# Optimization experiments

Hardware: AMD Instinct MI355X
Metric: run time of the kernel (lower is better)

Reference implementation:

```python
import jax, jax.numpy as jnp
import numpy as np

VEC, H, B, S = 768, 256, 64, 512


def setup_inputs() -> dict:
    key = jax.random.key(0)
    ks = jax.random.split(key, 8)
    sc = 0.02
    return {
        "output_1": jax.random.normal(ks[0], (B, S, VEC), dtype=jnp.float32),
        "output_2": jax.random.normal(ks[1], (B, S, VEC), dtype=jnp.float32),
        "mlp_w": jax.random.normal(ks[2], (H, VEC), dtype=jnp.float32) * sc,
        "mlp_b": jnp.zeros((H,), dtype=jnp.float32),
        "fd_w": jax.random.normal(ks[3], (H, 2 * H), dtype=jnp.float32) * sc,
        "fd_b": jnp.zeros((H,), dtype=jnp.float32),
        "ff_w": jax.random.normal(ks[4], (1, H), dtype=jnp.float32) * sc,
        "ff_b": jnp.zeros((1,), dtype=jnp.float32),
    }


def reference(output_1, output_2, mlp_w, mlp_b, fd_w, fd_b, ff_w, ff_b):
    # eval-mode forward of Bert_coss
    o1 = jax.nn.relu(output_1 @ mlp_w.T + mlp_b)        # [B,S,H]
    o2 = jax.nn.relu(output_2 @ mlp_w.T + mlp_b)        # [B,S,H]
    o1_doc = jnp.mean(o1, axis=1)                        # [B,H]
    o2_doc = jnp.mean(o2, axis=1)                        # [B,H]
    h = jax.nn.relu(jnp.concatenate([o1_doc, o2_doc], axis=1) @ fd_w.T + fd_b)
    out = jax.nn.sigmoid(jnp.squeeze(h @ ff_w.T + ff_b))  # [B]
    # append doc vectors as an extra token
    o1e = jnp.concatenate([o1, o1_doc[:, None, :]], axis=1)  # [B,S+1,H]
    o2e = jnp.concatenate([o2, o2_doc[:, None, :]], axis=1)  # [B,S+1,H]
    # graph_match: scores + softmax over dim=1; only last column is used downstream
    a = jnp.einsum('bsh,bth->bst', o1e, o2e)             # [B,S+1,S+1]
    a_x = jax.nn.softmax(a, axis=1)
    att = a_x[:, :, -1].T                                # [S+1,B]
    att = jnp.concatenate([att[:-1], out[None, :]], axis=0)  # [S+1,B]
    return att
```

## Files before the change

### kernel.cpp

```cpp
#include <hip/hip_runtime.h>
#include <hip/hip_bf16.h>
#include <math.h>

#define B_ 64
#define S_ 512
#define VEC_ 768
#define H_ 256
#define M_ (B_*S_)

typedef float floatx4 __attribute__((ext_vector_type(4)));
typedef __bf16 bf16x8 __attribute__((ext_vector_type(8)));
typedef __bf16 bf16x4 __attribute__((ext_vector_type(4)));

#define STRIDE 40

__global__ __launch_bounds__(256) void prep_kernel(
    const float* __restrict__ mlp_w, __bf16* __restrict__ wbf, float* __restrict__ sums)
{
  const int bid = blockIdx.x;
  if (bid < 192) {
    const int i = bid * 256 + threadIdx.x;
    const float4 v = ((const float4*)mlp_w)[i];
    bf16x4 b = { (__bf16)v.x, (__bf16)v.y, (__bf16)v.z, (__bf16)v.w };
    *(bf16x4*)&wbf[(size_t)i * 4] = b;
  } else {
    const int i = (bid - 192) * 256 + threadIdx.x;
    ((float4*)sums)[i] = make_float4(0.f, 0.f, 0.f, 0.f);
  }
}

__global__ __launch_bounds__(256) void gemm_doc_kernel(
    const float* __restrict__ out1, const float* __restrict__ out2,
    const __bf16* __restrict__ wbf, const float* __restrict__ mlp_b,
    __bf16* __restrict__ o1, float* __restrict__ sum1, float* __restrict__ sum2)
{
  __shared__ __align__(16) __bf16 As[128 * STRIDE];
  __shared__ __align__(16) __bf16 Bs[128 * STRIDE];

  const int tensor = blockIdx.z;
  const float* __restrict__ A = tensor ? out2 : out1;
  float* __restrict__ dsum = tensor ? sum2 : sum1;

  const int n0 = blockIdx.x * 128;
  const int m0 = blockIdx.y * 128;
  const int bidx = m0 >> 9;

  const int t = threadIdx.x;
  const int lane = t & 63;
  const int wave = t >> 6;
  const int q = lane >> 4;
  const int c = lane & 15;
  const int wm = (wave >> 1) * 64;
  const int wn = (wave & 1) * 64;

  floatx4 acc[4][4];
  for (int i = 0; i < 4; i++)
    for (int j = 0; j < 4; j++)
      acc[i][j] = (floatx4){0.f, 0.f, 0.f, 0.f};

  float4 aR[4];
  bf16x8 bR[2];

  {
    const float* Ab = &A[(size_t)m0 * VEC_];
    const __bf16* Wb = &wbf[(size_t)n0 * VEC_];
#pragma unroll
    for (int i = 0; i < 4; i++) {
      const int ch = t + i * 256;
      aR[i] = *(const float4*)&Ab[(size_t)(ch >> 3) * VEC_ + (ch & 7) * 4];
    }
#pragma unroll
    for (int i = 0; i < 2; i++) {
      const int ch = t + i * 256;
      bR[i] = *(const bf16x8*)&Wb[(size_t)(ch >> 2) * VEC_ + (ch & 3) * 8];
    }
  }

#pragma unroll 1
  for (int k0 = 0; k0 < VEC_; k0 += 32) {
#pragma unroll
    for (int i = 0; i < 4; i++) {
      const int ch = t + i * 256;
      bf16x4 v = { (__bf16)aR[i].x, (__bf16)aR[i].y, (__bf16)aR[i].z, (__bf16)aR[i].w };
      *(bf16x4*)&As[(ch >> 3) * STRIDE + (ch & 7) * 4] = v;
    }
#pragma unroll
    for (int i = 0; i < 2; i++) {
      const int ch = t + i * 256;
      *(bf16x8*)&Bs[(ch >> 2) * STRIDE + (ch & 3) * 8] = bR[i];
    }
    if (k0 + 32 < VEC_) {
      const float* Ab = &A[(size_t)m0 * VEC_ + k0 + 32];
      const __bf16* Wb = &wbf[(size_t)n0 * VEC_ + k0 + 32];
#pragma unroll
      for (int i = 0; i < 4; i++) {
        const int ch = t + i * 256;
        aR[i] = *(const float4*)&Ab[(size_t)(ch >> 3) * VEC_ + (ch & 7) * 4];
      }
#pragma unroll
      for (int i = 0; i < 2; i++) {
        const int ch = t + i * 256;
        bR[i] = *(const bf16x8*)&Wb[(size_t)(ch >> 2) * VEC_ + (ch & 3) * 8];
      }
    }
    __syncthreads();
    bf16x8 af[4], bfr[4];
#pragma unroll
    for (int i = 0; i < 4; i++) af[i]  = *(const bf16x8*)&As[(wm + i * 16 + c) * STRIDE + q * 8];
#pragma unroll
    for (int j = 0; j < 4; j++) bfr[j] = *(const bf16x8*)&Bs[(wn + j * 16 + c) * STRIDE + q * 8];
#pragma unroll
    for (int i = 0; i < 4; i++)
#pragma unroll
      for (int j = 0; j < 4; j++)
        acc[i][j] = __builtin_amdgcn_mfma_f32_16x16x32_bf16(af[i], bfr[j], acc[i][j], 0, 0, 0);
    __syncthreads();
  }

#pragma unroll
  for (int j = 0; j < 4; j++) {
    const int n = n0 + wn + j * 16 + c;
    const float bias = mlp_b[n];
    float colsum = 0.f;
#pragma unroll
    for (int i = 0; i < 4; i++) {
      const int mbase = m0 + wm + i * 16 + q * 4;
#pragma unroll
      for (int r = 0; r < 4; r++) {
        float v = acc[i][j][r] + bias;
        v = fmaxf(v, 0.f);
        colsum += v;
        if (tensor == 0) o1[(size_t)(mbase + r) * H_ + n] = (__bf16)v;
      }
    }
    colsum += __shfl_down(colsum, 32);
    colsum += __shfl_down(colsum, 16);
    if (lane < 16)
      atomicAdd(&dsum[bidx * H_ + n0 + wn + j * 16 + lane], colsum);
  }
}

__global__ __launch_bounds__(256) void logits_kernel(
    const __bf16* __restrict__ o1, const float* __restrict__ sum1,
    const float* __restrict__ sum2, float* __restrict__ lg)
{
  const int b = blockIdx.y;
  const int schunk = blockIdx.x;
  const int t = threadIdx.x, lane = t & 63, wave = t >> 6;
  __shared__ __align__(16) float o2d[256];
  if (t < 256) o2d[t] = sum2[b * H_ + t] * (1.f / 512.f);
  __syncthreads();
  const float4 w = ((const float4*)o2d)[lane];
  const int sbase = schunk * 64;
  for (int s = sbase + wave; s < sbase + 64; s += 4) {
    const bf16x4 x = *(const bf16x4*)&o1[((size_t)b * S_ + s) * H_ + lane * 4];
    float p = (float)x[0] * w.x + (float)x[1] * w.y + (float)x[2] * w.z + (float)x[3] * w.w;
    p += __shfl_down(p, 32); p += __shfl_down(p, 16); p += __shfl_down(p, 8);
    p += __shfl_down(p, 4);  p += __shfl_down(p, 2);  p += __shfl_down(p, 1);
    if (lane == 0) lg[b * 513 + s] = p;
  }
  if (schunk == 0 && wave == 0) {
    const float4 x = ((const float4*)&sum1[b * H_])[lane];
    float p = (x.x * w.x + x.y * w.y + x.z * w.z + x.w * w.w) * (1.f / 512.f);
    p += __shfl_down(p, 32); p += __shfl_down(p, 16); p += __shfl_down(p, 8);
    p += __shfl_down(p, 4);  p += __shfl_down(p, 2);  p += __shfl_down(p, 1);
    if (lane == 0) lg[b * 513 + 512] = p;
  }
}

__global__ __launch_bounds__(256) void softmax_head_kernel(
    const float* __restrict__ lg, const float* __restrict__ sum1, const float* __restrict__ sum2,
    const float* __restrict__ fd_w, const float* __restrict__ fd_b,
    const float* __restrict__ ff_w, const float* __restrict__ ff_b,
    float* __restrict__ out)
{
  const int b = blockIdx.x, t = threadIdx.x, lane = t & 63, wave = t >> 6;
  __shared__ __align__(16) float dc[512];
  __shared__ float sl[513];
  __shared__ float red[4], r1[4], r2[4];

  dc[t]       = sum1[b * H_ + t] * (1.f / 512.f);
  dc[t + 256] = sum2[b * H_ + t] * (1.f / 512.f);
  for (int i = t; i < 513; i += 256) sl[i] = lg[b * 513 + i];
  __syncthreads();
  const float4* wrow = (const float4*)&fd_w[(size_t)t * 512];
  const float4* dc4  = (const float4*)dc;
  float acc = 0.f;
  for (int k = 0; k < 128; k++) {
    const float4 w = wrow[k], d = dc4[k];
    acc += w.x * d.x + w.y * d.y + w.z * d.z + w.w * d.w;
  }
  const float h = fmaxf(acc + fd_b[t], 0.f);
  float part = ff_w[t] * h;
  part += __shfl_down(part, 32); part += __shfl_down(part, 16);
  part += __shfl_down(part, 8);  part += __shfl_down(part, 4);
  part += __shfl_down(part, 2);  part += __shfl_down(part, 1);
  if (lane == 0) red[wave] = part;

  float m = -1e30f;
  for (int i = t; i < 513; i += 256) m = fmaxf(m, sl[i]);
  m = fmaxf(m, __shfl_down(m, 32)); m = fmaxf(m, __shfl_down(m, 16));
  m = fmaxf(m, __shfl_down(m, 8));  m = fmaxf(m, __shfl_down(m, 4));
  m = fmaxf(m, __shfl_down(m, 2));  m = fmaxf(m, __shfl_down(m, 1));
  if (lane == 0) r1[wave] = m;
  __syncthreads();
  m = fmaxf(fmaxf(r1[0], r1[1]), fmaxf(r1[2], r1[3]));
  float psum = 0.f;
  for (int i = t; i < 513; i += 256) { const float e = expf(sl[i] - m); sl[i] = e; psum += e; }
  psum += __shfl_down(psum, 32); psum += __shfl_down(psum, 16); psum += __shfl_down(psum, 8);
  psum += __shfl_down(psum, 4);  psum += __shfl_down(psum, 2);  psum += __shfl_down(psum, 1);
  if (lane == 0) r2[wave] = psum;
  __syncthreads();
  const float inv = 1.f / (r2[0] + r2[1] + r2[2] + r2[3]);
  for (int s = t; s < 512; s += 256) out[s * 64 + b] = sl[s] * inv;
  if (t == 0) {
    const float tot = red[0] + red[1] + red[2] + red[3] + ff_b[0];
    out[(size_t)512 * 64 + b] = 1.f / (1.f + expf(-tot));
  }
}

extern "C" void kernel_launch(void* const* d_in, const int* in_sizes, int n_in,
                              void* d_out, int out_size, void* d_ws, size_t ws_size,
                              hipStream_t stream) {
  const float* out1  = (const float*)d_in[0];
  const float* out2  = (const float*)d_in[1];
  const float* mlp_w = (const float*)d_in[2];
  const float* mlp_b = (const float*)d_in[3];
  const float* fd_w  = (const float*)d_in[4];
  const float* fd_b  = (const float*)d_in[5];
  const float* ff_w  = (const float*)d_in[6];
  const float* ff_b  = (const float*)d_in[7];
  float* out = (float*)d_out;

  __bf16* o1  = (__bf16*)d_ws;
  __bf16* wbf = o1 + (size_t)M_ * H_;
  float*  s1  = (float*)(wbf + (size_t)H_ * VEC_);
  float*  s2  = s1 + B_ * H_;
  float*  lgw = s2 + B_ * H_;

  prep_kernel<<<224, 256, 0, stream>>>(mlp_w, wbf, s1);
  gemm_doc_kernel<<<dim3(2, 256, 2), 256, 0, stream>>>(out1, out2, wbf, mlp_b, o1, s1, s2);
  logits_kernel<<<dim3(8, B_), 256, 0, stream>>>(o1, s1, s2, lgw);
  softmax_head_kernel<<<B_, 256, 0, stream>>>(lgw, s1, s2, fd_w, fd_b, ff_w, ff_b, out);
}
```

Before: 284.2 us.

## Load GEMM fragments directly from global into registers, dropping LDS staging

The projection GEMM no longer stages A and W tiles through shared memory. Each wave reads its MFMA operand fragments straight from global memory, with a one-step register prefetch and a fully unrolled K loop, and the launch bounds now request two blocks per CU. This removes the LDS writes and reads and both barriers per K step. In exchange, the global loads are less coalesced, tiles are read redundantly across waves, and register pressure rises.

```diff
diff --git a/kernel.cpp b/kernel.cpp
--- a/kernel.cpp
+++ b/kernel.cpp
@@ -11,8 +11,6 @@
 typedef float floatx4 __attribute__((ext_vector_type(4)));
 typedef __bf16 bf16x8 __attribute__((ext_vector_type(8)));
 typedef __bf16 bf16x4 __attribute__((ext_vector_type(4)));
-
-#define STRIDE 40
 
 __global__ __launch_bounds__(256) void prep_kernel(
     const float* __restrict__ mlp_w, __bf16* __restrict__ wbf, float* __restrict__ sums)
@@ -29,14 +27,11 @@
   }
 }
 
-__global__ __launch_bounds__(256) void gemm_doc_kernel(
+__global__ __launch_bounds__(256, 2) void gemm_doc_kernel(
     const float* __restrict__ out1, const float* __restrict__ out2,
     const __bf16* __restrict__ wbf, const float* __restrict__ mlp_b,
     __bf16* __restrict__ o1, float* __restrict__ sum1, float* __restrict__ sum2)
 {
-  __shared__ __align__(16) __bf16 As[128 * STRIDE];
-  __shared__ __align__(16) __bf16 Bs[128 * STRIDE];
-
   const int tensor = blockIdx.z;
   const float* __restrict__ A = tensor ? out2 : out1;
   float* __restrict__ dsum = tensor ? sum2 : sum1;
@@ -45,76 +40,63 @@
   const int m0 = blockIdx.y * 128;
   const int bidx = m0 >> 9;
 
-  const int t = threadIdx.x;
-  const int lane = t & 63;
-  const int wave = t >> 6;
+  const int lane = threadIdx.x & 63;
+  const int wave = threadIdx.x >> 6;
   const int q = lane >> 4;
   const int c = lane & 15;
   const int wm = (wave >> 1) * 64;
   const int wn = (wave & 1) * 64;
 
+  const float* Ab[4];
+  const __bf16* Bb[4];
+#pragma unroll
+  for (int i = 0; i < 4; i++)
+    Ab[i] = A + (size_t)(m0 + wm + i * 16 + c) * VEC_ + q * 8;
+#pragma unroll
+  for (int j = 0; j < 4; j++)
+    Bb[j] = wbf + (size_t)(n0 + wn + j * 16 + c) * VEC_ + q * 8;
+
   floatx4 acc[4][4];
+#pragma unroll
   for (int i = 0; i < 4; i++)
+#pragma unroll
     for (int j = 0; j < 4; j++)
       acc[i][j] = (floatx4){0.f, 0.f, 0.f, 0.f};
 
-  float4 aR[4];
-  bf16x8 bR[2];
-
-  {
-    const float* Ab = &A[(size_t)m0 * VEC_];
-    const __bf16* Wb = &wbf[(size_t)n0 * VEC_];
-#pragma unroll
-    for (int i = 0; i < 4; i++) {
-      const int ch = t + i * 256;
-      aR[i] = *(const float4*)&Ab[(size_t)(ch >> 3) * VEC_ + (ch & 7) * 4];
+  float4 a0[4], a1[4], na0[4], na1[4];
+  bf16x8 b0[4], nb0[4];
+
+#pragma unroll
+  for (int i = 0; i < 4; i++) { a0[i] = *(const float4*)Ab[i]; a1[i] = *(const float4*)(Ab[i] + 4); }
+#pragma unroll
+  for (int j = 0; j < 4; j++) b0[j] = *(const bf16x8*)Bb[j];
+
+#pragma unroll
+  for (int kk = 0; kk < VEC_ / 32; kk++) {
+    const int kn = kk * 32 + 32;
+    if (kn < VEC_) {
+#pragma unroll
+      for (int i = 0; i < 4; i++) {
+        na0[i] = *(const float4*)(Ab[i] + kn);
+        na1[i] = *(const float4*)(Ab[i] + kn + 4);
+      }
+#pragma unroll
+      for (int j = 0; j < 4; j++) nb0[j] = *(const bf16x8*)(Bb[j] + kn);
     }
-#pragma unroll
-    for (int i = 0; i < 2; i++) {
-      const int ch = t + i * 256;
-      bR[i] = *(const bf16x8*)&Wb[(size_t)(ch >> 2) * VEC_ + (ch & 3) * 8];
-    }
-  }
-
-#pragma unroll 1
-  for (int k0 = 0; k0 < VEC_; k0 += 32) {
-#pragma unroll
-    for (int i = 0; i < 4; i++) {
-      const int ch = t + i * 256;
-      bf16x4 v = { (__bf16)aR[i].x, (__bf16)aR[i].y, (__bf16)aR[i].z, (__bf16)aR[i].w };
-      *(bf16x4*)&As[(ch >> 3) * STRIDE + (ch & 7) * 4] = v;
-    }
-#pragma unroll
-    for (int i = 0; i < 2; i++) {
-      const int ch = t + i * 256;
-      *(bf16x8*)&Bs[(ch >> 2) * STRIDE + (ch & 3) * 8] = bR[i];
-    }
-    if (k0 + 32 < VEC_) {
-      const float* Ab = &A[(size_t)m0 * VEC_ + k0 + 32];
-      const __bf16* Wb = &wbf[(size_t)n0 * VEC_ + k0 + 32];
-#pragma unroll
-      for (int i = 0; i < 4; i++) {
-        const int ch = t + i * 256;
-        aR[i] = *(const float4*)&Ab[(size_t)(ch >> 3) * VEC_ + (ch & 7) * 4];
-      }
-#pragma unroll
-      for (int i = 0; i < 2; i++) {
-        const int ch = t + i * 256;
-        bR[i] = *(const bf16x8*)&Wb[(size_t)(ch >> 2) * VEC_ + (ch & 3) * 8];
-      }
-    }
-    __syncthreads();
-    bf16x8 af[4], bfr[4];
-#pragma unroll
-    for (int i = 0; i < 4; i++) af[i]  = *(const bf16x8*)&As[(wm + i * 16 + c) * STRIDE + q * 8];
-#pragma unroll
-    for (int j = 0; j < 4; j++) bfr[j] = *(const bf16x8*)&Bs[(wn + j * 16 + c) * STRIDE + q * 8];
+    bf16x8 af[4];
 #pragma unroll
     for (int i = 0; i < 4; i++)
+      af[i] = (bf16x8){ (__bf16)a0[i].x, (__bf16)a0[i].y, (__bf16)a0[i].z, (__bf16)a0[i].w,
+                        (__bf16)a1[i].x, (__bf16)a1[i].y, (__bf16)a1[i].z, (__bf16)a1[i].w };
+#pragma unroll
+    for (int i = 0; i < 4; i++)
 #pragma unroll
       for (int j = 0; j < 4; j++)
-        acc[i][j] = __builtin_amdgcn_mfma_f32_16x16x32_bf16(af[i], bfr[j], acc[i][j], 0, 0, 0);
-    __syncthreads();
+        acc[i][j] = __builtin_amdgcn_mfma_f32_16x16x32_bf16(af[i], b0[j], acc[i][j], 0, 0, 0);
+#pragma unroll
+    for (int i = 0; i < 4; i++) { a0[i] = na0[i]; a1[i] = na1[i]; }
+#pragma unroll
+    for (int j = 0; j < 4; j++) b0[j] = nb0[j];
   }
 
 #pragma unroll
```

Measured after the change: 401.5 us. +41.3%, slower.

## Load GEMM tiles directly to LDS via global_load_lds with XOR swizzle

Applied to the files above, without the earlier changes.

Replaces the register-staged prefetch of A (fp32) and W (bf16) tiles with direct global-to-LDS loads. A is now kept as fp32 in LDS with an XOR-swizzled chunk layout and converted to bf16 at fragment-read time; B is unpadded. The register double-buffer is removed, so load latency is no longer overlapped with MFMA within a block. Instead, launch_bounds(256,4) requests higher occupancy to hide that latency across blocks. The fp32 A tile doubles LDS use for A, and the unpadded Bs layout may cause bank conflicts on fragment reads.

```diff
diff --git a/kernel.cpp b/kernel.cpp
--- a/kernel.cpp
+++ b/kernel.cpp
@@ -12,7 +12,11 @@
 typedef __bf16 bf16x8 __attribute__((ext_vector_type(8)));
 typedef __bf16 bf16x4 __attribute__((ext_vector_type(4)));
 
-#define STRIDE 40
+__device__ __forceinline__ void gl_lds16(const void* g, void* l) {
+  __builtin_amdgcn_global_load_lds(
+      (const __attribute__((address_space(1))) void*)g,
+      (__attribute__((address_space(3))) void*)l, 16, 0, 0);
+}
 
 __global__ __launch_bounds__(256) void prep_kernel(
     const float* __restrict__ mlp_w, __bf16* __restrict__ wbf, float* __restrict__ sums)
@@ -29,13 +33,13 @@
   }
 }
 
-__global__ __launch_bounds__(256) void gemm_doc_kernel(
+__global__ __launch_bounds__(256, 4) void gemm_doc_kernel(
     const float* __restrict__ out1, const float* __restrict__ out2,
     const __bf16* __restrict__ wbf, const float* __restrict__ mlp_b,
     __bf16* __restrict__ o1, float* __restrict__ sum1, float* __restrict__ sum2)
 {
-  __shared__ __align__(16) __bf16 As[128 * STRIDE];
-  __shared__ __align__(16) __bf16 Bs[128 * STRIDE];
+  __shared__ __align__(16) float  As[128 * 32];
+  __shared__ __align__(16) __bf16 Bs[128 * 32];
 
   const int tensor = blockIdx.z;
   const float* __restrict__ A = tensor ? out2 : out1;
@@ -53,62 +57,53 @@
   const int wm = (wave >> 1) * 64;
   const int wn = (wave & 1) * 64;
 
+  int arow[4], agch[4];
+#pragma unroll
+  for (int j = 0; j < 4; j++) {
+    const int s = wave * 256 + j * 64 + lane;
+    arow[j] = s >> 3;
+    agch[j] = (s & 7) ^ (arow[j] & 7);
+  }
+  int brow[2], bch[2];
+#pragma unroll
+  for (int j = 0; j < 2; j++) {
+    const int s = wave * 128 + j * 64 + lane;
+    brow[j] = s >> 2;
+    bch[j] = s & 3;
+  }
+
   floatx4 acc[4][4];
+#pragma unroll
   for (int i = 0; i < 4; i++)
+#pragma unroll
     for (int j = 0; j < 4; j++)
       acc[i][j] = (floatx4){0.f, 0.f, 0.f, 0.f};
 
-  float4 aR[4];
-  bf16x8 bR[2];
-
-  {
-    const float* Ab = &A[(size_t)m0 * VEC_];
-    const __bf16* Wb = &wbf[(size_t)n0 * VEC_];
-#pragma unroll
-    for (int i = 0; i < 4; i++) {
-      const int ch = t + i * 256;
-      aR[i] = *(const float4*)&Ab[(size_t)(ch >> 3) * VEC_ + (ch & 7) * 4];
-    }
-#pragma unroll
-    for (int i = 0; i < 2; i++) {
-      const int ch = t + i * 256;
-      bR[i] = *(const bf16x8*)&Wb[(size_t)(ch >> 2) * VEC_ + (ch & 3) * 8];
-    }
-  }
-
 #pragma unroll 1
   for (int k0 = 0; k0 < VEC_; k0 += 32) {
 #pragma unroll
+    for (int j = 0; j < 4; j++)
+      gl_lds16(&A[(size_t)(m0 + arow[j]) * VEC_ + k0 + agch[j] * 4],
+               &As[(wave * 256 + j * 64) * 4]);
+#pragma unroll
+    for (int j = 0; j < 2; j++)
+      gl_lds16(&wbf[(size_t)(n0 + brow[j]) * VEC_ + k0 + bch[j] * 8],
+               &Bs[(wave * 128 + j * 64) * 8]);
+    __syncthreads();
+
+    bf16x8 af[4], bfr[4];
+#pragma unroll
     for (int i = 0; i < 4; i++) {
-      const int ch = t + i * 256;
-      bf16x4 v = { (__bf16)aR[i].x, (__bf16)aR[i].y, (__bf16)aR[i].z, (__bf16)aR[i].w };
-      *(bf16x4*)&As[(ch >> 3) * STRIDE + (ch & 7) * 4] = v;
+      const int r = wm + i * 16 + c;
+      const int p0 = (2 * q) ^ (r & 7);
+      const floatx4 lo = *(const floatx4*)&As[r * 32 + p0 * 4];
+      const floatx4 hi = *(const floatx4*)&As[r * 32 + (p0 ^ 1) * 4];
+      af[i] = (bf16x8){ (__bf16)lo[0], (__bf16)lo[1], (__bf16)lo[2], (__bf16)lo[3],
+                        (__bf16)hi[0], (__bf16)hi[1], (__bf16)hi[2], (__bf16)hi[3] };
     }
 #pragma unroll
-    for (int i = 0; i < 2; i++) {
-      const int ch = t + i * 256;
-      *(bf16x8*)&Bs[(ch >> 2) * STRIDE + (ch & 3) * 8] = bR[i];
-    }
-    if (k0 + 32 < VEC_) {
-      const float* Ab = &A[(size_t)m0 * VEC_ + k0 + 32];
-      const __bf16* Wb = &wbf[(size_t)n0 * VEC_ + k0 + 32];
-#pragma unroll
-      for (int i = 0; i < 4; i++) {
-        const int ch = t + i * 256;
-        aR[i] = *(const float4*)&Ab[(size_t)(ch >> 3) * VEC_ + (ch & 7) * 4];
-      }
-#pragma unroll
-      for (int i = 0; i < 2; i++) {
-        const int ch = t + i * 256;
-        bR[i] = *(const bf16x8*)&Wb[(size_t)(ch >> 2) * VEC_ + (ch & 3) * 8];
-      }
-    }
-    __syncthreads();
-    bf16x8 af[4], bfr[4];
-#pragma unroll
-    for (int i = 0; i < 4; i++) af[i]  = *(const bf16x8*)&As[(wm + i * 16 + c) * STRIDE + q * 8];
-#pragma unroll
-    for (int j = 0; j < 4; j++) bfr[j] = *(const bf16x8*)&Bs[(wn + j * 16 + c) * STRIDE + q * 8];
+    for (int j = 0; j < 4; j++)
+      bfr[j] = *(const bf16x8*)&Bs[(wn + j * 16 + c) * 32 + q * 8];
 #pragma unroll
     for (int i = 0; i < 4; i++)
 #pragma unroll
```

After: 292.1 us. +2.8%, slower.
